# Optimization experiments

Hardware: AMD Instinct MI355X
Metric: run time of the kernel (lower is better)

Reference implementation:

```python
import jax, jax.numpy as jnp
import numpy as np

B, S, H, E, V = 64, 256, 1024, 256, 32000

def setup_inputs() -> dict:
    key = jax.random.key(0)
    ks = jax.random.split(key, 16)
    sc = 0.02
    return {
        'x': jax.random.randint(ks[0], (B, 1), 0, V),
        'dec_hs': jax.random.normal(ks[1], (1, B, H), jnp.float32),
        'enc_output': jax.random.normal(ks[2], (S, B, H), jnp.float32),
        'emb_table': jax.random.normal(ks[3], (V, E), jnp.float32) * sc,
        'w1_W': jax.random.normal(ks[4], (H, H), jnp.float32) * sc,
        'w1_b': jnp.zeros((H,), jnp.float32),
        'w2_W': jax.random.normal(ks[5], (H, H), jnp.float32) * sc,
        'w2_b': jnp.zeros((H,), jnp.float32),
        'v_W': jax.random.normal(ks[6], (1, H), jnp.float32) * sc,
        'v_b': jnp.zeros((1,), jnp.float32),
        'gru_W_ih': jax.random.normal(ks[7], (3 * H, H + E), jnp.float32) * sc,
        'gru_W_hh': jax.random.normal(ks[8], (3 * H, H), jnp.float32) * sc,
        'gru_b_ih': jnp.zeros((3 * H,), jnp.float32),
        'gru_b_hh': jnp.zeros((3 * H,), jnp.float32),
        'fc_W': jax.random.normal(ks[9], (V, H), jnp.float32) * sc,
        'fc_b': jnp.zeros((V,), jnp.float32),
    }

def reference(x, dec_hs, enc_output, emb_table, w1_W, w1_b, w2_W, w2_b,
              v_W, v_b, gru_W_ih, gru_W_hh, gru_b_ih, gru_b_hh, fc_W, fc_b):
    # ---- Bahdanau additive attention ----
    dec = jnp.transpose(dec_hs, (1, 0, 2))        # [B,1,H]
    enc = jnp.transpose(enc_output, (1, 0, 2))    # [B,S,H]
    feat = jnp.tanh(dec @ w1_W.T + w1_b + enc @ w2_W.T + w2_b)  # [B,S,H]
    scores = feat @ v_W.T + v_b                   # [B,S,1]
    attn = jax.nn.softmax(scores, axis=1)         # [B,S,1]
    context = jnp.sum(attn * enc, axis=1)         # [B,H]
    # ---- embedding lookup + concat ----
    emb = emb_table[x[:, 0]]                      # [B,E]
    gru_in = jnp.concatenate([context, emb], axis=-1)  # [B,H+E]
    # ---- single-step GRU (PyTorch gate convention) ----
    h = dec_hs[0]                                 # [B,H]
    gi = gru_in @ gru_W_ih.T + gru_b_ih           # [B,3H]
    gh = h @ gru_W_hh.T + gru_b_hh                # [B,3H]
    gi_r, gi_z, gi_n = jnp.split(gi, 3, axis=-1)
    gh_r, gh_z, gh_n = jnp.split(gh, 3, axis=-1)
    r = jax.nn.sigmoid(gi_r + gh_r)
    z = jax.nn.sigmoid(gi_z + gh_z)
    n = jnp.tanh(gi_n + r * gh_n)
    h_new = (1.0 - z) * n + z * h                 # [B,H]
    # ---- output projection ----
    fc_out = h_new @ fc_W.T + fc_b                # [B,V]
    return fc_out, h_new[None], attn
```

## Files before the change

kernel.cpp:

```cpp
#include <hip/hip_runtime.h>

#define BB 64
#define SS 256
#define HH 1024
#define EE 256
#define VV 32000

typedef unsigned short u16;
typedef __attribute__((ext_vector_type(4))) unsigned short u16x4;
typedef __attribute__((ext_vector_type(8))) short s16x8;
typedef __attribute__((ext_vector_type(4))) float f32x4;

typedef const void __attribute__((address_space(1)))* gas_p;
typedef void __attribute__((address_space(3)))* las_p;

__device__ __forceinline__ u16 f2bf(float f) {
  unsigned u = __builtin_bit_cast(unsigned, f);
  u += 0x7fffu + ((u >> 16) & 1u);
  return (u16)(u >> 16);
}
__device__ __forceinline__ float bf2f(u16 u) {
  return __builtin_bit_cast(float, ((unsigned)u) << 16);
}
__device__ __forceinline__ void gload16(const void* g, void* l) {
  __builtin_amdgcn_global_load_lds((gas_p)g, (las_p)l, 16, 0, 0);
}
#define MFMA16(a, b, c) __builtin_amdgcn_mfma_f32_16x16x32_bf16(a, b, c, 0, 0, 0)

__global__ __launch_bounds__(256) void k_convert(const float* __restrict__ enc,
    const float* __restrict__ w2, const float* __restrict__ dec,
    u16* __restrict__ Ap, u16* __restrict__ w2b, u16* __restrict__ hb) {
  int bid = blockIdx.x, t = threadIdx.x;
  const float* src;
  u16* dst;
  if (bid < BB * SS) {
    int b = bid >> 8, s = bid & 255;
    src = enc + (size_t)(s * BB + b) * HH;
    dst = Ap + (size_t)bid * HH;
  } else if (bid < BB * SS + HH) {
    int r = bid - BB * SS;
    src = w2 + (size_t)r * HH;
    dst = w2b + (size_t)r * HH;
  } else {
    int b = bid - (BB * SS + HH);
    src = dec + (size_t)b * HH;
    dst = hb + (size_t)b * HH;
  }
  f32x4 v = *(const f32x4*)(src + t * 4);
  u16x4 o = { f2bf(v[0]), f2bf(v[1]), f2bf(v[2]), f2bf(v[3]) };
  *(u16x4*)(dst + t * 4) = o;
}

__global__ __launch_bounds__(256) void k_dbmm(const u16* __restrict__ hb,
    const float* __restrict__ w1, float* __restrict__ dbp) {
  int kc = blockIdx.y;
  int kb = kc * 128;
  int n0 = blockIdx.x * 128;
  __shared__ u16 Ws[2][128 * 32];
  int t = threadIdx.x, lane = t & 63, w = t >> 6;
  int wm = w >> 1, wn = w & 1, l15 = lane & 15, lg = lane >> 4;
  f32x4 acc[2][4] = {};
  int kx = (lg ^ ((l15 >> 1) & 3)) * 8;
  int wrow = t >> 1, wh = t & 1;
  int xr = (wrow >> 1) & 3;
  int s0 = (2 * wh) ^ xr, s1 = (2 * wh + 1) ^ xr;
  const float* gW = w1 + (size_t)(n0 + wrow) * HH + kb + wh * 16;
  const u16* gA = hb + kb + lg * 8;
  f32x4 c0 = *(const f32x4*)(gW);
  f32x4 c1 = *(const f32x4*)(gW + 4);
  f32x4 c2 = *(const f32x4*)(gW + 8);
  f32x4 c3 = *(const f32x4*)(gW + 12);
  s16x8 a0 = *(const s16x8*)(gA + (size_t)(wm * 32 + l15) * HH);
  s16x8 a1 = *(const s16x8*)(gA + (size_t)(wm * 32 + 16 + l15) * HH);
  {
    u16* lw = &Ws[0][wrow * 32];
    u16x4 o0 = { f2bf(c0[0]), f2bf(c0[1]), f2bf(c0[2]), f2bf(c0[3]) };
    u16x4 o1 = { f2bf(c1[0]), f2bf(c1[1]), f2bf(c1[2]), f2bf(c1[3]) };
    u16x4 o2 = { f2bf(c2[0]), f2bf(c2[1]), f2bf(c2[2]), f2bf(c2[3]) };
    u16x4 o3 = { f2bf(c3[0]), f2bf(c3[1]), f2bf(c3[2]), f2bf(c3[3]) };
    *(u16x4*)(lw + s0 * 8) = o0; *(u16x4*)(lw + s0 * 8 + 4) = o1;
    *(u16x4*)(lw + s1 * 8) = o2; *(u16x4*)(lw + s1 * 8 + 4) = o3;
  }
  __syncthreads();
  for (int it = 0; it < 4; ++it) {
    int nlast = (it < 3);
    f32x4 n0v, n1v, n2v, n3v;
    s16x8 an0, an1;
    if (nlast) {
      int k1 = (it + 1) * 32;
      n0v = *(const f32x4*)(gW + k1);
      n1v = *(const f32x4*)(gW + k1 + 4);
      n2v = *(const f32x4*)(gW + k1 + 8);
      n3v = *(const f32x4*)(gW + k1 + 12);
      an0 = *(const s16x8*)(gA + (size_t)(wm * 32 + l15) * HH + k1);
      an1 = *(const s16x8*)(gA + (size_t)(wm * 32 + 16 + l15) * HH + k1);
    }
    const u16* wb = Ws[it & 1];
    s16x8 bfr[4];
#pragma unroll
    for (int ni = 0; ni < 4; ++ni)
      bfr[ni] = *(const s16x8*)&wb[(wn * 64 + ni * 16 + l15) * 32 + kx];
#pragma unroll
    for (int ni = 0; ni < 4; ++ni) {
      acc[0][ni] = MFMA16(a0, bfr[ni], acc[0][ni]);
      acc[1][ni] = MFMA16(a1, bfr[ni], acc[1][ni]);
    }
    if (nlast) {
      u16* lw = &Ws[(it + 1) & 1][wrow * 32];
      u16x4 o0 = { f2bf(n0v[0]), f2bf(n0v[1]), f2bf(n0v[2]), f2bf(n0v[3]) };
      u16x4 o1 = { f2bf(n1v[0]), f2bf(n1v[1]), f2bf(n1v[2]), f2bf(n1v[3]) };
      u16x4 o2 = { f2bf(n2v[0]), f2bf(n2v[1]), f2bf(n2v[2]), f2bf(n2v[3]) };
      u16x4 o3 = { f2bf(n3v[0]), f2bf(n3v[1]), f2bf(n3v[2]), f2bf(n3v[3]) };
      *(u16x4*)(lw + s0 * 8) = o0; *(u16x4*)(lw + s0 * 8 + 4) = o1;
      *(u16x4*)(lw + s1 * 8) = o2; *(u16x4*)(lw + s1 * 8 + 4) = o3;
      a0 = an0; a1 = an1;
    }
    __syncthreads();
  }
  float* Pb = dbp + (size_t)kc * 64 * HH;
#pragma unroll
  for (int mi = 0; mi < 2; ++mi)
#pragma unroll
    for (int ni = 0; ni < 4; ++ni)
#pragma unroll
      for (int r = 0; r < 4; ++r) {
        int m = wm * 32 + mi * 16 + lg * 4 + r;
        int n = n0 + wn * 64 + ni * 16 + l15;
        Pb[(size_t)m * HH + n] = acc[mi][ni][r];
      }
}

__global__ __launch_bounds__(256) void k_biggemm(const u16* __restrict__ Ap,
    const u16* __restrict__ Bw, const float* __restrict__ w1b,
    const float* __restrict__ w2bias, const float* __restrict__ dbp,
    const float* __restrict__ vW, float* __restrict__ sp) {
  __shared__ u16 As[128 * 32];
  __shared__ u16 Bs[128 * 32];
  __shared__ float sc[2][128];
  int bid = blockIdx.x;
  int mt = ((bid >> 6) << 3) | (bid & 7);
  int nt = (bid >> 3) & 7;
  int t = threadIdx.x, lane = t & 63, w = t >> 6;
  int wm = w >> 1, wn = w & 1, l15 = lane & 15, lg = lane >> 4;
  int m0 = mt * 128, n0 = nt * 128;
  int b = m0 >> 8;
  f32x4 acc[4][4] = {};
  int srow = w * 32 + (lane >> 2);
  int sq = ((lane & 3) ^ ((lane >> 3) & 3)) * 8;
  const u16* gA = Ap + (size_t)(m0 + srow) * HH + sq;
  const u16* gB = Bw + (size_t)(n0 + srow) * HH + sq;
  u16* lA = As + w * 32 * 32;
  u16* lB = Bs + w * 32 * 32;
  int kx = (lg ^ ((l15 >> 1) & 3)) * 8;
  for (int it = 0; it < 32; ++it) {
    int k0 = it * 32;
    gload16(gA + k0, lA);
    gload16(gA + (size_t)16 * HH + k0, lA + 16 * 32);
    gload16(gB + k0, lB);
    gload16(gB + (size_t)16 * HH + k0, lB + 16 * 32);
    __syncthreads();
    s16x8 af[4], bfr[4];
#pragma unroll
    for (int mi = 0; mi < 4; ++mi)
      af[mi] = *(const s16x8*)&As[(wm * 64 + mi * 16 + l15) * 32 + kx];
#pragma unroll
    for (int ni = 0; ni < 4; ++ni)
      bfr[ni] = *(const s16x8*)&Bs[(wn * 64 + ni * 16 + l15) * 32 + kx];
#pragma unroll
    for (int mi = 0; mi < 4; ++mi)
#pragma unroll
      for (int ni = 0; ni < 4; ++ni)
        acc[mi][ni] = MFMA16(af[mi], bfr[ni], acc[mi][ni]);
    __syncthreads();
  }
  const float* vv = vW + n0;
  float dbs[4];
#pragma unroll
  for (int ni = 0; ni < 4; ++ni) {
    int nl = wn * 64 + ni * 16 + l15;
    int n = n0 + nl;
    float s = w1b[n] + w2bias[n];
#pragma unroll
    for (int p = 0; p < 8; ++p) s += dbp[(size_t)p * 64 * HH + (size_t)b * HH + n];
    dbs[ni] = s;
  }
#pragma unroll
  for (int mi = 0; mi < 4; ++mi) {
#pragma unroll
    for (int r = 0; r < 4; ++r) {
      float p = 0.f;
#pragma unroll
      for (int ni = 0; ni < 4; ++ni) {
        int nl = wn * 64 + ni * 16 + l15;
        p += tanhf(acc[mi][ni][r] + dbs[ni]) * vv[nl];
      }
      p += __shfl_xor(p, 1); p += __shfl_xor(p, 2);
      p += __shfl_xor(p, 4); p += __shfl_xor(p, 8);
      if (l15 == 0) sc[wn][wm * 64 + mi * 16 + lg * 4 + r] = p;
    }
  }
  __syncthreads();
  if (t < 128) sp[(size_t)(m0 + t) * 8 + nt] = sc[0][t] + sc[1][t];
}

__global__ __launch_bounds__(256) void k_softmax(const float* __restrict__ sp,
    const float* __restrict__ vb, float* __restrict__ attn) {
  int b = blockIdx.x, t = threadIdx.x;
  int lane = t & 63, w = t >> 6;
  const float* row = sp + (size_t)(b * SS + t) * 8;
  f32x4 a = *(const f32x4*)row;
  f32x4 c = *(const f32x4*)(row + 4);
  float score = a[0] + a[1] + a[2] + a[3] + c[0] + c[1] + c[2] + c[3] + vb[0];
  __shared__ float rmax[4], rsum[4];
  float m = score;
  for (int mk = 1; mk < 64; mk <<= 1) m = fmaxf(m, __shfl_xor(m, mk));
  if (lane == 0) rmax[w] = m;
  __syncthreads();
  m = fmaxf(fmaxf(rmax[0], rmax[1]), fmaxf(rmax[2], rmax[3]));
  float e = expf(score - m);
  float ssum = e;
  for (int mk = 1; mk < 64; mk <<= 1) ssum += __shfl_xor(ssum, mk);
  if (lane == 0) rsum[w] = ssum;
  __syncthreads();
  float tot = rsum[0] + rsum[1] + rsum[2] + rsum[3];
  attn[(size_t)b * SS + t] = e / tot;
}

__global__ __launch_bounds__(256) void k_context(const float* __restrict__ attn,
    const u16* __restrict__ Ap, float* __restrict__ ctxp) {
  int sc = blockIdx.x, b = blockIdx.y, t = threadIdx.x;
  __shared__ float at[64];
  if (t < 64) at[t] = attn[(size_t)b * SS + sc * 64 + t];
  __syncthreads();
  const u16* base = Ap + (size_t)(b * SS + sc * 64) * HH + t * 4;
  float a0 = 0.f, a1 = 0.f, a2 = 0.f, a3 = 0.f;
#pragma unroll 4
  for (int s = 0; s < 64; ++s) {
    u16x4 v = *(const u16x4*)(base + (size_t)s * HH);
    float av = at[s];
    a0 += av * bf2f(v[0]); a1 += av * bf2f(v[1]);
    a2 += av * bf2f(v[2]); a3 += av * bf2f(v[3]);
  }
  f32x4 o = { a0, a1, a2, a3 };
  *(f32x4*)&ctxp[(size_t)(b * 4 + sc) * HH + t * 4] = o;
}

__global__ __launch_bounds__(256) void k_ctxcomb(const float* __restrict__ ctxp,
    const int* __restrict__ x, const float* __restrict__ emb,
    u16* __restrict__ gin) {
  int b = blockIdx.x, t = threadIdx.x;
  f32x4 s = {0.f, 0.f, 0.f, 0.f};
#pragma unroll
  for (int p = 0; p < 4; ++p)
    s += *(const f32x4*)&ctxp[(size_t)(b * 4 + p) * HH + t * 4];
  u16x4 o = { f2bf(s[0]), f2bf(s[1]), f2bf(s[2]), f2bf(s[3]) };
  *(u16x4*)(gin + (size_t)b * 1280 + t * 4) = o;
  int xb = x[b];
  gin[(size_t)b * 1280 + HH + t] = f2bf(emb[(size_t)xb * EE + t]);
}

__global__ __launch_bounds__(256) void k_gru(const u16* __restrict__ gin,
    const u16* __restrict__ hb, const float* __restrict__ Wih,
    const float* __restrict__ Whh, float* __restrict__ P) {
  int y = blockIdx.y;
  int z = (y >= 5);
  const u16* Ab = z ? hb : gin;
  const float* Wf = z ? Whh : Wih;
  int K = z ? HH : (HH + EE);
  int kb = (z ? (y - 5) : y) * 256;
  int n0 = blockIdx.x * 128;
  __shared__ u16 Ws[2][128 * 32];
  int t = threadIdx.x, lane = t & 63, w = t >> 6;
  int wm = w >> 1, wn = w & 1, l15 = lane & 15, lg = lane >> 4;
  f32x4 acc[2][4] = {};
  int kx = (lg ^ ((l15 >> 1) & 3)) * 8;
  int wrow = t >> 1, wh = t & 1;
  int xr = (wrow >> 1) & 3;
  int s0 = (2 * wh) ^ xr, s1 = (2 * wh + 1) ^ xr;
  const float* gW = Wf + (size_t)(n0 + wrow) * K + kb + wh * 16;
  const u16* gA = Ab + kb + lg * 8;
  f32x4 c0 = *(const f32x4*)(gW);
  f32x4 c1 = *(const f32x4*)(gW + 4);
  f32x4 c2 = *(const f32x4*)(gW + 8);
  f32x4 c3 = *(const f32x4*)(gW + 12);
  s16x8 a0 = *(const s16x8*)(gA + (size_t)(wm * 32 + l15) * K);
  s16x8 a1 = *(const s16x8*)(gA + (size_t)(wm * 32 + 16 + l15) * K);
  {
    u16* lw = &Ws[0][wrow * 32];
    u16x4 o0 = { f2bf(c0[0]), f2bf(c0[1]), f2bf(c0[2]), f2bf(c0[3]) };
    u16x4 o1 = { f2bf(c1[0]), f2bf(c1[1]), f2bf(c1[2]), f2bf(c1[3]) };
    u16x4 o2 = { f2bf(c2[0]), f2bf(c2[1]), f2bf(c2[2]), f2bf(c2[3]) };
    u16x4 o3 = { f2bf(c3[0]), f2bf(c3[1]), f2bf(c3[2]), f2bf(c3[3]) };
    *(u16x4*)(lw + s0 * 8) = o0; *(u16x4*)(lw + s0 * 8 + 4) = o1;
    *(u16x4*)(lw + s1 * 8) = o2; *(u16x4*)(lw + s1 * 8 + 4) = o3;
  }
  __syncthreads();
  for (int it = 0; it < 8; ++it) {
    int nlast = (it < 7);
    f32x4 n0v, n1v, n2v, n3v;
    s16x8 an0, an1;
    if (nlast) {
      int k1 = (it + 1) * 32;
      n0v = *(const f32x4*)(gW + k1);
      n1v = *(const f32x4*)(gW + k1 + 4);
      n2v = *(const f32x4*)(gW + k1 + 8);
      n3v = *(const f32x4*)(gW + k1 + 12);
      an0 = *(const s16x8*)(gA + (size_t)(wm * 32 + l15) * K + k1);
      an1 = *(const s16x8*)(gA + (size_t)(wm * 32 + 16 + l15) * K + k1);
    }
    const u16* wb = Ws[it & 1];
    s16x8 bfr[4];
#pragma unroll
    for (int ni = 0; ni < 4; ++ni)
      bfr[ni] = *(const s16x8*)&wb[(wn * 64 + ni * 16 + l15) * 32 + kx];
#pragma unroll
    for (int ni = 0; ni < 4; ++ni) {
      acc[0][ni] = MFMA16(a0, bfr[ni], acc[0][ni]);
      acc[1][ni] = MFMA16(a1, bfr[ni], acc[1][ni]);
    }
    if (nlast) {
      u16* lw = &Ws[(it + 1) & 1][wrow * 32];
      u16x4 o0 = { f2bf(n0v[0]), f2bf(n0v[1]), f2bf(n0v[2]), f2bf(n0v[3]) };
      u16x4 o1 = { f2bf(n1v[0]), f2bf(n1v[1]), f2bf(n1v[2]), f2bf(n1v[3]) };
      u16x4 o2 = { f2bf(n2v[0]), f2bf(n2v[1]), f2bf(n2v[2]), f2bf(n2v[3]) };
      u16x4 o3 = { f2bf(n3v[0]), f2bf(n3v[1]), f2bf(n3v[2]), f2bf(n3v[3]) };
      *(u16x4*)(lw + s0 * 8) = o0; *(u16x4*)(lw + s0 * 8 + 4) = o1;
      *(u16x4*)(lw + s1 * 8) = o2; *(u16x4*)(lw + s1 * 8 + 4) = o3;
      a0 = an0; a1 = an1;
    }
    __syncthreads();
  }
  float* Pb = P + (size_t)y * 64 * 3072;
#pragma unroll
  for (int mi = 0; mi < 2; ++mi)
#pragma unroll
    for (int ni = 0; ni < 4; ++ni)
#pragma unroll
      for (int r = 0; r < 4; ++r) {
        int m = wm * 32 + mi * 16 + lg * 4 + r;
        int n = n0 + wn * 64 + ni * 16 + l15;
        Pb[(size_t)m * 3072 + n] = acc[mi][ni][r];
      }
}

__global__ __launch_bounds__(256) void k_gates(const float* __restrict__ P,
    const float* __restrict__ bih, const float* __restrict__ bhh,
    const float* __restrict__ dec, float* __restrict__ hn_out,
    u16* __restrict__ hnb) {
  int b = blockIdx.x, t = threadIdx.x;
#pragma unroll
  for (int j = 0; j < 4; ++j) {
    int h = t + j * 256;
    float gir = 0.f, giz = 0.f, gin_ = 0.f, ghr = 0.f, ghz = 0.f, ghn = 0.f;
#pragma unroll
    for (int y = 0; y < 5; ++y) {
      const float* r = P + (size_t)(y * 64 + b) * 3072;
      gir += r[h]; giz += r[h + 1024]; gin_ += r[h + 2048];
    }
#pragma unroll
    for (int y = 0; y < 4; ++y) {
      const float* r = P + (size_t)((5 + y) * 64 + b) * 3072;
      ghr += r[h]; ghz += r[h + 1024]; ghn += r[h + 2048];
    }
    float rr = 1.f / (1.f + expf(-(gir + bih[h] + ghr + bhh[h])));
    float zz = 1.f / (1.f + expf(-(giz + bih[1024 + h] + ghz + bhh[1024 + h])));
    float nn = tanhf(gin_ + bih[2048 + h] + rr * (ghn + bhh[2048 + h]));
    float hv = dec[(size_t)b * HH + h];
    float hnew = (1.f - zz) * nn + zz * hv;
    hn_out[(size_t)b * HH + h] = hnew;
    hnb[(size_t)b * HH + h] = f2bf(hnew);
  }
}

__global__ __launch_bounds__(256) void k_fc(const u16* __restrict__ hnb,
    const float* __restrict__ W, const float* __restrict__ bias,
    float* __restrict__ out) {
  int n0 = blockIdx.x * 64;
  __shared__ u16 Ws[2][64 * 32];
  int t = threadIdx.x, lane = t & 63, w = t >> 6;
  int wm = w >> 1, wn = w & 1, l15 = lane & 15, lg = lane >> 4;
  f32x4 acc[2][2] = {};
  int kx = (lg ^ ((l15 >> 1) & 3)) * 8;
  int wrow = t >> 2;
  int sq = ((t & 3) ^ ((t >> 3) & 3)) * 8;
  const float* gW = W + (size_t)(n0 + wrow) * HH + (t & 3) * 8;
  const u16* gA = hnb + lg * 8;
  f32x4 c0 = *(const f32x4*)(gW);
  f32x4 c1 = *(const f32x4*)(gW + 4);
  s16x8 a0 = *(const s16x8*)(gA + (size_t)(wm * 32 + l15) * HH);
  s16x8 a1 = *(const s16x8*)(gA + (size_t)(wm * 32 + 16 + l15) * HH);
  {
    u16* lw = &Ws[0][wrow * 32 + sq];
    u16x4 o0 = { f2bf(c0[0]), f2bf(c0[1]), f2bf(c0[2]), f2bf(c0[3]) };
    u16x4 o1 = { f2bf(c1[0]), f2bf(c1[1]), f2bf(c1[2]), f2bf(c1[3]) };
    *(u16x4*)(lw) = o0; *(u16x4*)(lw + 4) = o1;
  }
  __syncthreads();
  for (int it = 0; it < 32; ++it) {
    int nlast = (it < 31);
    f32x4 n0v, n1v;
    s16x8 an0, an1;
    if (nlast) {
      int k1 = (it + 1) * 32;
      n0v = *(const f32x4*)(gW + k1);
      n1v = *(const f32x4*)(gW + k1 + 4);
      an0 = *(const s16x8*)(gA + (size_t)(wm * 32 + l15) * HH + k1);
      an1 = *(const s16x8*)(gA + (size_t)(wm * 32 + 16 + l15) * HH + k1);
    }
    const u16* wb = Ws[it & 1];
    s16x8 bfr[2];
#pragma unroll
    for (int ni = 0; ni < 2; ++ni)
      bfr[ni] = *(const s16x8*)&wb[(wn * 32 + ni * 16 + l15) * 32 + kx];
#pragma unroll
    for (int ni = 0; ni < 2; ++ni) {
      acc[0][ni] = MFMA16(a0, bfr[ni], acc[0][ni]);
      acc[1][ni] = MFMA16(a1, bfr[ni], acc[1][ni]);
    }
    if (nlast) {
      u16* lw = &Ws[(it + 1) & 1][wrow * 32 + sq];
      u16x4 o0 = { f2bf(n0v[0]), f2bf(n0v[1]), f2bf(n0v[2]), f2bf(n0v[3]) };
      u16x4 o1 = { f2bf(n1v[0]), f2bf(n1v[1]), f2bf(n1v[2]), f2bf(n1v[3]) };
      *(u16x4*)(lw) = o0; *(u16x4*)(lw + 4) = o1;
      a0 = an0; a1 = an1;
    }
    __syncthreads();
  }
#pragma unroll
  for (int mi = 0; mi < 2; ++mi)
#pragma unroll
    for (int ni = 0; ni < 2; ++ni)
#pragma unroll
      for (int r = 0; r < 4; ++r) {
        int m = wm * 32 + mi * 16 + lg * 4 + r;
        int n = n0 + wn * 32 + ni * 16 + l15;
        out[(size_t)m * VV + n] = acc[mi][ni][r] + bias[n];
      }
}

extern "C" void kernel_launch(void* const* d_in, const int* in_sizes, int n_in,
                              void* d_out, int out_size, void* d_ws, size_t ws_size,
                              hipStream_t stream) {
  const int*   x      = (const int*)   d_in[0];
  const float* dec    = (const float*) d_in[1];
  const float* enc    = (const float*) d_in[2];
  const float* emb    = (const float*) d_in[3];
  const float* w1     = (const float*) d_in[4];
  const float* w1b    = (const float*) d_in[5];
  const float* w2     = (const float*) d_in[6];
  const float* w2bias = (const float*) d_in[7];
  const float* vW     = (const float*) d_in[8];
  const float* vb     = (const float*) d_in[9];
  const float* Wih    = (const float*) d_in[10];
  const float* Whh    = (const float*) d_in[11];
  const float* bih    = (const float*) d_in[12];
  const float* bhh    = (const float*) d_in[13];
  const float* fcW    = (const float*) d_in[14];
  const float* fcb    = (const float*) d_in[15];
  float* out = (float*)d_out;
  char* ws = (char*)d_ws;
  u16*   Ap    = (u16*)(ws);
  u16*   w2b   = (u16*)(ws + 33554432);
  u16*   hb    = (u16*)(ws + 35651584);
  u16*   gin   = (u16*)(ws + 35782656);
  u16*   hnb   = (u16*)(ws + 35946496);
  float* sp    = (float*)(ws + 36339712);
  float* P     = (float*)(ws + 36864000);
  float* dbp   = P;
  float* ctxp  = P + 524288;
  float* hn   = out + 2048000;
  float* attn = out + 2113536;

  k_convert<<<BB * SS + HH + BB, 256, 0, stream>>>(enc, w2, dec, Ap, w2b, hb);
  k_dbmm<<<dim3(8, 8), 256, 0, stream>>>(hb, w1, dbp);
  k_biggemm<<<1024, 256, 0, stream>>>(Ap, w2b, w1b, w2bias, dbp, vW, sp);
  k_softmax<<<BB, 256, 0, stream>>>(sp, vb, attn);
  k_context<<<dim3(4, BB), 256, 0, stream>>>(attn, Ap, ctxp);
  k_ctxcomb<<<BB, 256, 0, stream>>>(ctxp, x, emb, gin);
  k_gru<<<dim3(24, 9), 256, 0, stream>>>(gin, hb, Wih, Whh, P);
  k_gates<<<BB, 256, 0, stream>>>(P, bih, bhh, dec, hn, hnb);
  k_fc<<<500, 256, 0, stream>>>(hnb, fcW, fcb, out);
}
```

Baseline: 148.9 us.

## Double GEMM K-tile with XOR swizzle and fuse softmax into context kernel

The attention score GEMM now stages 64-wide K slices per iteration with a new 8-slot XOR LDS swizzle. This halves the loop trip count and barrier count at the cost of doubling shared memory per block. Softmax is fused into the context-weighted-sum kernel: each of 8 blocks per batch recomputes the softmax and handles 32 sequence rows. This removes one kernel launch and the attn round trip, and the context reduction kernel now sums 8 partials.

```diff
diff --git a/kernel.cpp b/kernel.cpp
--- a/kernel.cpp
+++ b/kernel.cpp
@@ -134,8 +134,8 @@
     const u16* __restrict__ Bw, const float* __restrict__ w1b,
     const float* __restrict__ w2bias, const float* __restrict__ dbp,
     const float* __restrict__ vW, float* __restrict__ sp) {
-  __shared__ u16 As[128 * 32];
-  __shared__ u16 Bs[128 * 32];
+  __shared__ u16 As[128 * 64];
+  __shared__ u16 Bs[128 * 64];
   __shared__ float sc[2][128];
   int bid = blockIdx.x;
   int mt = ((bid >> 6) << 3) | (bid & 7);
@@ -145,32 +145,42 @@
   int m0 = mt * 128, n0 = nt * 128;
   int b = m0 >> 8;
   f32x4 acc[4][4] = {};
-  int srow = w * 32 + (lane >> 2);
-  int sq = ((lane & 3) ^ ((lane >> 3) & 3)) * 8;
-  const u16* gA = Ap + (size_t)(m0 + srow) * HH + sq;
-  const u16* gB = Bw + (size_t)(n0 + srow) * HH + sq;
-  u16* lA = As + w * 32 * 32;
-  u16* lB = Bs + w * 32 * 32;
-  int kx = (lg ^ ((l15 >> 1) & 3)) * 8;
-  for (int it = 0; it < 32; ++it) {
-    int k0 = it * 32;
-    gload16(gA + k0, lA);
-    gload16(gA + (size_t)16 * HH + k0, lA + 16 * 32);
-    gload16(gB + k0, lB);
-    gload16(gB + (size_t)16 * HH + k0, lB + 16 * 32);
+  int srow = w * 32 + (lane >> 3);
+  int cswz = ((lane & 7) ^ (lane >> 3)) * 8;
+  const u16* gA = Ap + (size_t)(m0 + srow) * HH + cswz;
+  const u16* gB = Bw + (size_t)(n0 + srow) * HH + cswz;
+  u16* lA = As + w * 32 * 64;
+  u16* lB = Bs + w * 32 * 64;
+  for (int it = 0; it < 16; ++it) {
+    int k0 = it * 64;
+#pragma unroll
+    for (int i = 0; i < 4; ++i)
+      gload16(gA + (size_t)i * 8 * HH + k0, lA + i * 8 * 64);
+#pragma unroll
+    for (int i = 0; i < 4; ++i)
+      gload16(gB + (size_t)i * 8 * HH + k0, lB + i * 8 * 64);
     __syncthreads();
-    s16x8 af[4], bfr[4];
-#pragma unroll
-    for (int mi = 0; mi < 4; ++mi)
-      af[mi] = *(const s16x8*)&As[(wm * 64 + mi * 16 + l15) * 32 + kx];
-#pragma unroll
-    for (int ni = 0; ni < 4; ++ni)
-      bfr[ni] = *(const s16x8*)&Bs[(wn * 64 + ni * 16 + l15) * 32 + kx];
-#pragma unroll
-    for (int mi = 0; mi < 4; ++mi)
-#pragma unroll
-      for (int ni = 0; ni < 4; ++ni)
-        acc[mi][ni] = MFMA16(af[mi], bfr[ni], acc[mi][ni]);
+#pragma unroll
+    for (int kk = 0; kk < 2; ++kk) {
+      s16x8 af[4], bfr[4];
+#pragma unroll
+      for (int mi = 0; mi < 4; ++mi) {
+        int row = wm * 64 + mi * 16 + l15;
+        int slot = (kk * 4 + lg) ^ (row & 7);
+        af[mi] = *(const s16x8*)&As[row * 64 + slot * 8];
+      }
+#pragma unroll
+      for (int ni = 0; ni < 4; ++ni) {
+        int row = wn * 64 + ni * 16 + l15;
+        int slot = (kk * 4 + lg) ^ (row & 7);
+        bfr[ni] = *(const s16x8*)&Bs[row * 64 + slot * 8];
+      }
+#pragma unroll
+      for (int mi = 0; mi < 4; ++mi)
+#pragma unroll
+        for (int ni = 0; ni < 4; ++ni)
+          acc[mi][ni] = MFMA16(af[mi], bfr[ni], acc[mi][ni]);
+    }
     __syncthreads();
   }
   const float* vv = vW + n0;
@@ -203,15 +213,16 @@
   if (t < 128) sp[(size_t)(m0 + t) * 8 + nt] = sc[0][t] + sc[1][t];
 }
 
-__global__ __launch_bounds__(256) void k_softmax(const float* __restrict__ sp,
-    const float* __restrict__ vb, float* __restrict__ attn) {
-  int b = blockIdx.x, t = threadIdx.x;
+__global__ __launch_bounds__(256) void k_ctxsm(const float* __restrict__ sp,
+    const float* __restrict__ vb, const u16* __restrict__ Ap,
+    float* __restrict__ attn, float* __restrict__ ctxp) {
+  int sc = blockIdx.x, b = blockIdx.y, t = threadIdx.x;
   int lane = t & 63, w = t >> 6;
   const float* row = sp + (size_t)(b * SS + t) * 8;
   f32x4 a = *(const f32x4*)row;
   f32x4 c = *(const f32x4*)(row + 4);
   float score = a[0] + a[1] + a[2] + a[3] + c[0] + c[1] + c[2] + c[3] + vb[0];
-  __shared__ float rmax[4], rsum[4];
+  __shared__ float rmax[4], rsum[4], at[SS];
   float m = score;
   for (int mk = 1; mk < 64; mk <<= 1) m = fmaxf(m, __shfl_xor(m, mk));
   if (lane == 0) rmax[w] = m;
@@ -223,26 +234,21 @@
   if (lane == 0) rsum[w] = ssum;
   __syncthreads();
   float tot = rsum[0] + rsum[1] + rsum[2] + rsum[3];
-  attn[(size_t)b * SS + t] = e / tot;
-}
-
-__global__ __launch_bounds__(256) void k_context(const float* __restrict__ attn,
-    const u16* __restrict__ Ap, float* __restrict__ ctxp) {
-  int sc = blockIdx.x, b = blockIdx.y, t = threadIdx.x;
-  __shared__ float at[64];
-  if (t < 64) at[t] = attn[(size_t)b * SS + sc * 64 + t];
-  __syncthreads();
-  const u16* base = Ap + (size_t)(b * SS + sc * 64) * HH + t * 4;
+  float av = e / tot;
+  at[t] = av;
+  if (sc == 0) attn[(size_t)b * SS + t] = av;
+  __syncthreads();
+  const u16* base = Ap + (size_t)(b * SS + sc * 32) * HH + t * 4;
   float a0 = 0.f, a1 = 0.f, a2 = 0.f, a3 = 0.f;
 #pragma unroll 4
-  for (int s = 0; s < 64; ++s) {
+  for (int s = 0; s < 32; ++s) {
     u16x4 v = *(const u16x4*)(base + (size_t)s * HH);
-    float av = at[s];
-    a0 += av * bf2f(v[0]); a1 += av * bf2f(v[1]);
-    a2 += av * bf2f(v[2]); a3 += av * bf2f(v[3]);
+    float w_ = at[sc * 32 + s];
+    a0 += w_ * bf2f(v[0]); a1 += w_ * bf2f(v[1]);
+    a2 += w_ * bf2f(v[2]); a3 += w_ * bf2f(v[3]);
   }
   f32x4 o = { a0, a1, a2, a3 };
-  *(f32x4*)&ctxp[(size_t)(b * 4 + sc) * HH + t * 4] = o;
+  *(f32x4*)&ctxp[(size_t)(b * 8 + sc) * HH + t * 4] = o;
 }
 
 __global__ __launch_bounds__(256) void k_ctxcomb(const float* __restrict__ ctxp,
@@ -251,8 +257,8 @@
   int b = blockIdx.x, t = threadIdx.x;
   f32x4 s = {0.f, 0.f, 0.f, 0.f};
 #pragma unroll
-  for (int p = 0; p < 4; ++p)
-    s += *(const f32x4*)&ctxp[(size_t)(b * 4 + p) * HH + t * 4];
+  for (int p = 0; p < 8; ++p)
+    s += *(const f32x4*)&ctxp[(size_t)(b * 8 + p) * HH + t * 4];
   u16x4 o = { f2bf(s[0]), f2bf(s[1]), f2bf(s[2]), f2bf(s[3]) };
   *(u16x4*)(gin + (size_t)b * 1280 + t * 4) = o;
   int xb = x[b];
@@ -474,8 +480,7 @@
   k_convert<<<BB * SS + HH + BB, 256, 0, stream>>>(enc, w2, dec, Ap, w2b, hb);
   k_dbmm<<<dim3(8, 8), 256, 0, stream>>>(hb, w1, dbp);
   k_biggemm<<<1024, 256, 0, stream>>>(Ap, w2b, w1b, w2bias, dbp, vW, sp);
-  k_softmax<<<BB, 256, 0, stream>>>(sp, vb, attn);
-  k_context<<<dim3(4, BB), 256, 0, stream>>>(attn, Ap, ctxp);
+  k_ctxsm<<<dim3(8, BB), 256, 0, stream>>>(sp, vb, Ap, attn, ctxp);
   k_ctxcomb<<<BB, 256, 0, stream>>>(ctxp, x, emb, gin);
   k_gru<<<dim3(24, 9), 256, 0, stream>>>(gin, hb, Wih, Whh, P);
   k_gates<<<BB, 256, 0, stream>>>(P, bih, bhh, dec, hn, hnb);
```

Result: faster. 145.9 us (-2.0%).
